# Kernel optimization log

Measured on AMD Instinct MI355X. Metric: run time of the kernel, lower is better.

The kernel has to match this reference:

```python
import jax, jax.numpy as jnp
import numpy as np

TEMP = 0.5
WEIGHT = (0.4, 0.3, 0.3)


def _l2norm(x):
    n = jnp.linalg.norm(x, axis=-1, keepdims=True)
    return x / jnp.maximum(n, 1e-12)


def _forward(st_i, st_j, car_i, car_j, pl_i, pl_j, gt_labels,
             cen_st, cen_car, cen_pl, conc):
    w = jnp.asarray(WEIGHT, dtype=st_i.dtype)[:, None, None]  # [3,1,1]
    feats = [jnp.concatenate([_l2norm(a), _l2norm(b)], axis=0)
             for a, b in ((st_i, st_j), (car_i, car_j), (pl_i, pl_j))]  # each [N,D]
    sims = jnp.stack([f @ f.T for f in feats])  # [3,N,N]
    wmask = jnp.where(sims == 0, jnp.zeros_like(w), w)
    wsim = (sims * wmask).sum(0) / (wmask.sum(0) + 1e-12)  # [N,N]
    e = jnp.exp(wsim / TEMP)
    N = e.shape[0]
    B = N // 2
    idx = jnp.arange(N)
    pos = e[idx, (idx + B) % N]  # positive_mask gather: one positive per row
    # negative_mask excludes diagonal and the positive -> row sum minus both
    neg_sum = e.sum(-1) - e[idx, idx] - pos
    loss = (-jnp.log(pos / (pos + neg_sum))).mean()

    # prototype branch: gt_labels covers all C clusters, unique set == arange(C)
    labels = gt_labels[:, 0]  # [N]
    C = cen_st.shape[0]
    k = jnp.arange(C - 1)
    neg_ids = k[None, :] + (k[None, :] >= labels[:, None]).astype(k.dtype)  # sorted ids != label
    proto_ids = jnp.concatenate([labels[:, None], neg_ids], axis=1)  # [N,C], col 0 = positive
    logits = jnp.stack([
        jnp.take_along_axis(f @ c.T, proto_ids, axis=1)
        for f, c in zip(feats, (cen_st, cen_car, cen_pl))])  # [3,N,C]
    temp_proto = conc[:, proto_ids]  # [3,N,C]
    logits = logits / (temp_proto + 1e-12)
    w2 = jnp.where((temp_proto == 0) | (logits == 0), jnp.zeros_like(w), w)
    logits_w = (logits * w2).sum(0) / (w2.sum(0) + 1e-12)  # [N,C]
    # CrossEntropyLoss(mean) with target class 0 for every row
    loss_proto = (-jax.nn.log_softmax(logits_w, axis=-1)[:, 0]).mean()
    return loss + loss_proto


def setup_inputs() -> dict:
    key = jax.random.key(0)
    ks = jax.random.split(key, 12)
    B, D, C = 2048, 128, 512
    N = 2 * B
    inp = {}
    names = ['st_feat_i', 'st_feat_j', 'car_feat_i', 'car_feat_j',
             'plate_feat_i', 'plate_feat_j']
    for i, nm in enumerate(names):
        inp[nm] = jax.random.normal(ks[i], (B, D), dtype=jnp.float32)
    # labels covering all C clusters so torch.unique(gt_labels) == arange(C)
    labels = jnp.tile(jnp.arange(C, dtype=jnp.int32), N // C)
    labels = jax.random.permutation(ks[6], labels)
    inp['gt_labels'] = labels[:, None]
    inp['st_centroids'] = jax.random.normal(ks[7], (C, D), dtype=jnp.float32)
    inp['car_centroids'] = jax.random.normal(ks[8], (C, D), dtype=jnp.float32)
    inp['plate_centroids'] = jax.random.normal(ks[9], (C, D), dtype=jnp.float32)
    inp['concentration'] = jax.random.uniform(ks[10], (3, C), dtype=jnp.float32,
                                              minval=0.1, maxval=1.0)
    return inp


def reference(st_feat_i, st_feat_j, car_feat_i, car_feat_j,
              plate_feat_i, plate_feat_j, gt_labels,
              st_centroids, car_centroids, plate_centroids, concentration):
    return _forward(st_feat_i, st_feat_j, car_feat_i, car_feat_j,
                    plate_feat_i, plate_feat_j, gt_labels,
                    st_centroids, car_centroids, plate_centroids, concentration)
```

## Files before the change

kernel.cpp:

```cpp
#include <hip/hip_runtime.h>
#include <hip/hip_bf16.h>
#include <math.h>

#define BB 2048
#define NN 4096
#define DD 128
#define CC 512

typedef __attribute__((ext_vector_type(8))) short bf16x8;
typedef __attribute__((ext_vector_type(4))) float f32x4;

__global__ void k_norm(const float* __restrict__ si, const float* __restrict__ sj,
                       const float* __restrict__ ci, const float* __restrict__ cj,
                       const float* __restrict__ pi, const float* __restrict__ pj,
                       __hip_bfloat16* __restrict__ fbf) {
  const int row = blockIdx.x;
  const int m   = blockIdx.y;
  const float* src;
  float sqw;
  if (m == 0)      { src = (row < BB) ? si : sj; sqw = 0.632455532033676f; }
  else if (m == 1) { src = (row < BB) ? ci : cj; sqw = 0.547722557505166f; }
  else             { src = (row < BB) ? pi : pj; sqw = 0.547722557505166f; }
  const int r = (row < BB) ? row : row - BB;
  const float2* s2 = (const float2*)(src + (size_t)r * DD);
  const int t = threadIdx.x;
  float2 v = s2[t];
  float ss = v.x * v.x + v.y * v.y;
  #pragma unroll
  for (int k = 32; k >= 1; k >>= 1) ss += __shfl_xor(ss, k);
  const float inv = sqw / fmaxf(sqrtf(ss), 1e-12f);
  __hip_bfloat16* db = fbf + (size_t)m * NN * DD + (size_t)row * DD;
  db[2 * t]     = __float2bfloat16(v.x * inv);
  db[2 * t + 1] = __float2bfloat16(v.y * inv);
}

__global__ void k_prep(const float* __restrict__ cst, const float* __restrict__ cca,
                       const float* __restrict__ cpl, const float* __restrict__ conc,
                       __hip_bfloat16* __restrict__ cbf) {
  const int row = blockIdx.x;
  const int m   = blockIdx.y;
  const float* src = (m == 0) ? cst : (m == 1) ? cca : cpl;
  const float sqw = (m == 0) ? 0.632455532033676f : 0.547722557505166f;
  const float sc  = sqw / (conc[m * CC + row] + 1e-12f);
  const float2* s2 = (const float2*)(src + (size_t)row * DD);
  const int t = threadIdx.x;
  float2 v = s2[t];
  __hip_bfloat16* db = cbf + (size_t)m * CC * DD + (size_t)row * DD;
  db[2 * t]     = __float2bfloat16(v.x * sc);
  db[2 * t + 1] = __float2bfloat16(v.y * sc);
}

__global__ __launch_bounds__(256, 3) void k_sim(const __hip_bfloat16* __restrict__ fbf,
                                                float* __restrict__ rowsum,
                                                float* __restrict__ pos_e,
                                                float* __restrict__ diag_e) {
  __shared__ bf16x8 As[1024];
  __shared__ bf16x8 Bs[1024];

  int tB = blockIdx.x;
  int by = 0;
  while (tB >= 32 - by) { tB -= 32 - by; ++by; }
  const int bx = by + tB;
  const bool diag = (by == bx);
  const int rowBase = by * 128;
  const int colBase = bx * 128;

  const int tid  = threadIdx.x;
  const int lane = tid & 63;
  const int wid  = tid >> 6;
  const int wr   = wid >> 1, wc = wid & 1;
  const int l15  = lane & 15;
  const int kg   = lane >> 4;

  const int srow = tid >> 3;
  const int kc   = tid & 7;
  const int sc   = kc ^ (srow & 7);

  f32x4 acc[4][4] = {};
  bf16x8 ra[4], rb[4];

  {
    const __hip_bfloat16* F = fbf;
    #pragma unroll
    for (int q = 0; q < 4; ++q) {
      ra[q] = *(const bf16x8*)(F + (size_t)(rowBase + q * 32 + srow) * DD + kc * 8);
      if (!diag)
        rb[q] = *(const bf16x8*)(F + (size_t)(colBase + q * 32 + srow) * DD + kc * 8);
    }
  }

  for (int t = 0; t < 6; ++t) {
    #pragma unroll
    for (int q = 0; q < 4; ++q) {
      As[(q * 32 + srow) * 8 + sc] = ra[q];
      if (!diag) Bs[(q * 32 + srow) * 8 + sc] = rb[q];
    }
    __syncthreads();

    if (t < 5) {
      const __hip_bfloat16* F = fbf + (size_t)((t + 1) >> 1) * NN * DD + ((t + 1) & 1) * 64;
      #pragma unroll
      for (int q = 0; q < 4; ++q) {
        ra[q] = *(const bf16x8*)(F + (size_t)(rowBase + q * 32 + srow) * DD + kc * 8);
        if (!diag)
          rb[q] = *(const bf16x8*)(F + (size_t)(colBase + q * 32 + srow) * DD + kc * 8);
      }
    }

    const bf16x8* Bsrc = diag ? As : Bs;
    #pragma unroll
    for (int ks2 = 0; ks2 < 2; ++ks2) {
      bf16x8 a[4], b[4];
      const int ch = (ks2 * 4 + kg) ^ (l15 & 7);
      #pragma unroll
      for (int ti = 0; ti < 4; ++ti)
        a[ti] = As[(wr * 64 + ti * 16 + l15) * 8 + ch];
      #pragma unroll
      for (int tj = 0; tj < 4; ++tj)
        b[tj] = Bsrc[(wc * 64 + tj * 16 + l15) * 8 + ch];
      #pragma unroll
      for (int ti = 0; ti < 4; ++ti)
        #pragma unroll
        for (int tj = 0; tj < 4; ++tj)
          acc[ti][tj] = __builtin_amdgcn_mfma_f32_16x16x32_bf16(a[ti], b[tj], acc[ti][tj], 0, 0, 0);
    }
    __syncthreads();
  }

  float csum[4] = {0.f, 0.f, 0.f, 0.f};
  #pragma unroll
  for (int ti = 0; ti < 4; ++ti) {
    #pragma unroll
    for (int j = 0; j < 4; ++j) {
      const int i = rowBase + wr * 64 + ti * 16 + kg * 4 + j;
      float rsum = 0.f;
      #pragma unroll
      for (int tj = 0; tj < 4; ++tj) {
        const int jcol = colBase + wc * 64 + tj * 16 + l15;
        const float e = expf(2.0f * acc[ti][tj][j]);
        rsum += e;
        csum[tj] += e;
        if (diag) {
          if (jcol == i) diag_e[i] = e;
        } else if (jcol == ((i + BB) & (NN - 1))) {
          pos_e[i] = e;
          pos_e[jcol] = e;
        }
      }
      #pragma unroll
      for (int msk = 8; msk >= 1; msk >>= 1) rsum += __shfl_xor(rsum, msk);
      if (l15 == 0) atomicAdd(&rowsum[i], rsum);
    }
  }
  if (!diag) {
    #pragma unroll
    for (int tj = 0; tj < 4; ++tj) {
      float v = csum[tj];
      v += __shfl_xor(v, 16);
      v += __shfl_xor(v, 32);
      if (lane < 16) atomicAdd(&rowsum[colBase + wc * 64 + tj * 16 + l15], v);
    }
  }
}

__global__ __launch_bounds__(256) void k_pmm(const __hip_bfloat16* __restrict__ fbf,
                                             const __hip_bfloat16* __restrict__ cbf,
                                             float* __restrict__ Z, int rowOff) {
  const int tid  = threadIdx.x;
  const int lane = tid & 63;
  const int wid  = tid >> 6;
  const int wr   = wid >> 1, wc = wid & 1;
  const int rowBase = rowOff + blockIdx.y * 64 + wr * 32;
  const int colBase = blockIdx.x * 64 + wc * 32;
  const int l15 = lane & 15;
  const int kg  = lane >> 4;

  f32x4 acc[2][2] = {};
  bf16x8 abuf[2][2], bbuf[2][2];

  {
    const int koff = kg * 8;
    #pragma unroll
    for (int ti = 0; ti < 2; ++ti) {
      abuf[0][ti] = *(const bf16x8*)(fbf + (size_t)(rowBase + ti * 16 + l15) * DD + koff);
      bbuf[0][ti] = *(const bf16x8*)(cbf + (size_t)(colBase + ti * 16 + l15) * DD + koff);
    }
  }
  #pragma unroll
  for (int ks = 0; ks < 12; ++ks) {
    const int cur = ks & 1, nxt = cur ^ 1;
    if (ks < 11) {
      const int k1 = ks + 1;
      const int koff = (k1 & 3) * 32 + kg * 8;
      const __hip_bfloat16* F  = fbf + (size_t)(k1 >> 2) * NN * DD + koff;
      const __hip_bfloat16* Cm = cbf + (size_t)(k1 >> 2) * CC * DD + koff;
      #pragma unroll
      for (int ti = 0; ti < 2; ++ti) {
        abuf[nxt][ti] = *(const bf16x8*)(F  + (size_t)(rowBase + ti * 16 + l15) * DD);
        bbuf[nxt][ti] = *(const bf16x8*)(Cm + (size_t)(colBase + ti * 16 + l15) * DD);
      }
    }
    #pragma unroll
    for (int ti = 0; ti < 2; ++ti)
      #pragma unroll
      for (int tj = 0; tj < 2; ++tj)
        acc[ti][tj] = __builtin_amdgcn_mfma_f32_16x16x32_bf16(abuf[cur][ti], bbuf[cur][tj], acc[ti][tj], 0, 0, 0);
  }

  #pragma unroll
  for (int ti = 0; ti < 2; ++ti) {
    #pragma unroll
    for (int j = 0; j < 4; ++j) {
      const int r = rowBase + ti * 16 + kg * 4 + j - rowOff;
      #pragma unroll
      for (int tj = 0; tj < 2; ++tj) {
        const int c = colBase + tj * 16 + l15;
        Z[(size_t)r * CC + c] = acc[ti][tj][j];
      }
    }
  }
}

__global__ __launch_bounds__(256) void k_smax(const float* __restrict__ Z,
                                              const int* __restrict__ labels,
                                              float* __restrict__ lossB, int rowOff) {
  const int tid  = threadIdx.x;
  const int lane = tid & 63;
  const int rloc = blockIdx.x * 4 + (tid >> 6);
  const int row  = rowOff + rloc;
  const float4* zr = (const float4*)(Z + (size_t)rloc * CC);
  const float4 a = zr[lane * 2];
  const float4 b = zr[lane * 2 + 1];
  float mx = fmaxf(fmaxf(fmaxf(a.x, a.y), fmaxf(a.z, a.w)),
                   fmaxf(fmaxf(b.x, b.y), fmaxf(b.z, b.w)));
  #pragma unroll
  for (int k = 32; k >= 1; k >>= 1) mx = fmaxf(mx, __shfl_xor(mx, k));
  float se = expf(a.x - mx) + expf(a.y - mx) + expf(a.z - mx) + expf(a.w - mx)
           + expf(b.x - mx) + expf(b.y - mx) + expf(b.z - mx) + expf(b.w - mx);
  #pragma unroll
  for (int k = 32; k >= 1; k >>= 1) se += __shfl_xor(se, k);
  if (lane == 0) {
    const float zlab = Z[(size_t)rloc * CC + labels[row]];
    lossB[row] = mx + logf(se) - zlab;
  }
}

__global__ void k_final(const float* __restrict__ rowsum, const float* __restrict__ pos_e,
                        const float* __restrict__ diag_e, const float* __restrict__ lossB,
                        float* __restrict__ out) {
  __shared__ float redA[4], redB[4];
  const int tid = threadIdx.x;
  float sa = 0.f, sb = 0.f;
  for (int i = tid; i < NN; i += 256) {
    sa += logf(rowsum[i] - diag_e[i]) - logf(pos_e[i]);
    sb += lossB[i];
  }
  const int lane = tid & 63, wv = tid >> 6;
  #pragma unroll
  for (int k = 32; k >= 1; k >>= 1) { sa += __shfl_xor(sa, k); sb += __shfl_xor(sb, k); }
  if (lane == 0) { redA[wv] = sa; redB[wv] = sb; }
  __syncthreads();
  if (tid == 0) {
    const float la = redA[0] + redA[1] + redA[2] + redA[3];
    const float lb = redB[0] + redB[1] + redB[2] + redB[3];
    out[0] = la / (float)NN + lb / (float)NN;
  }
}

extern "C" void kernel_launch(void* const* d_in, const int* in_sizes, int n_in,
                              void* d_out, int out_size, void* d_ws, size_t ws_size,
                              hipStream_t stream) {
  (void)in_sizes; (void)n_in; (void)out_size; (void)ws_size;
  const float* si  = (const float*)d_in[0];
  const float* sj  = (const float*)d_in[1];
  const float* ci  = (const float*)d_in[2];
  const float* cj  = (const float*)d_in[3];
  const float* pi  = (const float*)d_in[4];
  const float* pj  = (const float*)d_in[5];
  const int*   lab = (const int*)d_in[6];
  const float* cst = (const float*)d_in[7];
  const float* cca = (const float*)d_in[8];
  const float* cpl = (const float*)d_in[9];
  const float* cnc = (const float*)d_in[10];

  float* ws     = (float*)d_ws;
  float* Z      = ws;
  float* rowsum = Z + (size_t)BB * CC;
  float* pos_e  = rowsum + NN;
  float* diag_e = pos_e + NN;
  float* lossB  = diag_e + NN;
  __hip_bfloat16* fbf = (__hip_bfloat16*)(lossB + NN);
  __hip_bfloat16* cbf = fbf + (size_t)3 * NN * DD;

  hipMemsetAsync(rowsum, 0, NN * sizeof(float), stream);

  k_norm<<<dim3(NN, 3), 64, 0, stream>>>(si, sj, ci, cj, pi, pj, fbf);
  k_prep<<<dim3(CC, 3), 64, 0, stream>>>(cst, cca, cpl, cnc, cbf);
  k_sim<<<528, 256, 0, stream>>>(fbf, rowsum, pos_e, diag_e);
  k_pmm<<<dim3(CC / 64, BB / 64), 256, 0, stream>>>(fbf, cbf, Z, 0);
  k_smax<<<BB / 4, 256, 0, stream>>>(Z, lab, lossB, 0);
  k_pmm<<<dim3(CC / 64, BB / 64), 256, 0, stream>>>(fbf, cbf, Z, BB);
  k_smax<<<BB / 4, 256, 0, stream>>>(Z, lab, lossB, BB);
  k_final<<<1, 256, 0, stream>>>(rowsum, pos_e, diag_e, lossB, (float*)d_out);
}
```

Baseline: 134.2 us.

## Fuse prototype matmul with softmax cross-entropy and merge norm/prep kernels

Replaces the two-pass prototype path (matmul writing a logits matrix Z, then a separate softmax pass, run twice over row halves) with one kernel where each block computes 16 rows by all 512 centroids in registers and does the max/sum-exp/label pick in place via shuffles and shared memory. This drops the Z round-trip through global memory and cuts four launches down to one. Separately, the feature normalization and centroid prep kernels are merged into a single launch using 4 rows per 256-thread block. The fused kernel loses the double-buffered loads and launches only 256 blocks, each reading the full centroid set, so latency hiding and occupancy may be weaker.

New measurement: 127.9 us. -4.7%, faster.

```diff
diff --git a/kernel.cpp b/kernel.cpp
--- a/kernel.cpp
+++ b/kernel.cpp
@@ -10,44 +10,42 @@
 typedef __attribute__((ext_vector_type(8))) short bf16x8;
 typedef __attribute__((ext_vector_type(4))) float f32x4;
 
-__global__ void k_norm(const float* __restrict__ si, const float* __restrict__ sj,
-                       const float* __restrict__ ci, const float* __restrict__ cj,
-                       const float* __restrict__ pi, const float* __restrict__ pj,
-                       __hip_bfloat16* __restrict__ fbf) {
-  const int row = blockIdx.x;
+__global__ __launch_bounds__(256) void k_normprep(
+    const float* __restrict__ si, const float* __restrict__ sj,
+    const float* __restrict__ ci, const float* __restrict__ cj,
+    const float* __restrict__ pi, const float* __restrict__ pj,
+    const float* __restrict__ cst, const float* __restrict__ cca,
+    const float* __restrict__ cpl, const float* __restrict__ conc,
+    __hip_bfloat16* __restrict__ fbf, __hip_bfloat16* __restrict__ cbf) {
   const int m   = blockIdx.y;
-  const float* src;
-  float sqw;
-  if (m == 0)      { src = (row < BB) ? si : sj; sqw = 0.632455532033676f; }
-  else if (m == 1) { src = (row < BB) ? ci : cj; sqw = 0.547722557505166f; }
-  else             { src = (row < BB) ? pi : pj; sqw = 0.547722557505166f; }
-  const int r = (row < BB) ? row : row - BB;
-  const float2* s2 = (const float2*)(src + (size_t)r * DD);
-  const int t = threadIdx.x;
-  float2 v = s2[t];
-  float ss = v.x * v.x + v.y * v.y;
-  #pragma unroll
-  for (int k = 32; k >= 1; k >>= 1) ss += __shfl_xor(ss, k);
-  const float inv = sqw / fmaxf(sqrtf(ss), 1e-12f);
-  __hip_bfloat16* db = fbf + (size_t)m * NN * DD + (size_t)row * DD;
-  db[2 * t]     = __float2bfloat16(v.x * inv);
-  db[2 * t + 1] = __float2bfloat16(v.y * inv);
-}
-
-__global__ void k_prep(const float* __restrict__ cst, const float* __restrict__ cca,
-                       const float* __restrict__ cpl, const float* __restrict__ conc,
-                       __hip_bfloat16* __restrict__ cbf) {
-  const int row = blockIdx.x;
-  const int m   = blockIdx.y;
-  const float* src = (m == 0) ? cst : (m == 1) ? cca : cpl;
+  const int tid = threadIdx.x;
+  const int w   = tid >> 6;
+  const int t   = tid & 63;
   const float sqw = (m == 0) ? 0.632455532033676f : 0.547722557505166f;
-  const float sc  = sqw / (conc[m * CC + row] + 1e-12f);
-  const float2* s2 = (const float2*)(src + (size_t)row * DD);
-  const int t = threadIdx.x;
-  float2 v = s2[t];
-  __hip_bfloat16* db = cbf + (size_t)m * CC * DD + (size_t)row * DD;
-  db[2 * t]     = __float2bfloat16(v.x * sc);
-  db[2 * t + 1] = __float2bfloat16(v.y * sc);
+  if (blockIdx.x < NN / 4) {
+    const int row = blockIdx.x * 4 + w;
+    const float* src;
+    if (m == 0)      src = (row < BB) ? si : sj;
+    else if (m == 1) src = (row < BB) ? ci : cj;
+    else             src = (row < BB) ? pi : pj;
+    const int r = (row < BB) ? row : row - BB;
+    float2 v = ((const float2*)(src + (size_t)r * DD))[t];
+    float ss = v.x * v.x + v.y * v.y;
+    #pragma unroll
+    for (int k = 32; k >= 1; k >>= 1) ss += __shfl_xor(ss, k);
+    const float inv = sqw / fmaxf(sqrtf(ss), 1e-12f);
+    __hip_bfloat16* db = fbf + (size_t)m * NN * DD + (size_t)row * DD;
+    db[2 * t]     = __float2bfloat16(v.x * inv);
+    db[2 * t + 1] = __float2bfloat16(v.y * inv);
+  } else {
+    const int crow = (blockIdx.x - NN / 4) * 4 + w;
+    const float* src = (m == 0) ? cst : (m == 1) ? cca : cpl;
+    const float sc = sqw / (conc[m * CC + crow] + 1e-12f);
+    float2 v = ((const float2*)(src + (size_t)crow * DD))[t];
+    __hip_bfloat16* db = cbf + (size_t)m * CC * DD + (size_t)crow * DD;
+    db[2 * t]     = __float2bfloat16(v.x * sc);
+    db[2 * t + 1] = __float2bfloat16(v.y * sc);
+  }
 }
 
 __global__ __launch_bounds__(256, 3) void k_sim(const __hip_bfloat16* __restrict__ fbf,
@@ -163,85 +161,77 @@
   }
 }
 
-__global__ __launch_bounds__(256) void k_pmm(const __hip_bfloat16* __restrict__ fbf,
-                                             const __hip_bfloat16* __restrict__ cbf,
-                                             float* __restrict__ Z, int rowOff) {
+__global__ __launch_bounds__(256) void k_proto2(const __hip_bfloat16* __restrict__ fbf,
+                                                const __hip_bfloat16* __restrict__ cbf,
+                                                const int* __restrict__ labels,
+                                                float* __restrict__ lossB) {
+  __shared__ int   slab[16];
+  __shared__ float wmax[4][16], wsum[4][16], zlab[16];
   const int tid  = threadIdx.x;
   const int lane = tid & 63;
-  const int wid  = tid >> 6;
-  const int wr   = wid >> 1, wc = wid & 1;
-  const int rowBase = rowOff + blockIdx.y * 64 + wr * 32;
-  const int colBase = blockIdx.x * 64 + wc * 32;
-  const int l15 = lane & 15;
-  const int kg  = lane >> 4;
-
-  f32x4 acc[2][2] = {};
-  bf16x8 abuf[2][2], bbuf[2][2];
-
-  {
-    const int koff = kg * 8;
-    #pragma unroll
-    for (int ti = 0; ti < 2; ++ti) {
-      abuf[0][ti] = *(const bf16x8*)(fbf + (size_t)(rowBase + ti * 16 + l15) * DD + koff);
-      bbuf[0][ti] = *(const bf16x8*)(cbf + (size_t)(colBase + ti * 16 + l15) * DD + koff);
-    }
-  }
+  const int w    = tid >> 6;
+  const int l15  = lane & 15;
+  const int kg   = lane >> 4;
+  const int row0 = blockIdx.x * 16;
+
+  if (tid < 16) slab[tid] = labels[row0 + tid];
+  __syncthreads();
+
+  f32x4 acc[8] = {};
   #pragma unroll
   for (int ks = 0; ks < 12; ++ks) {
-    const int cur = ks & 1, nxt = cur ^ 1;
-    if (ks < 11) {
-      const int k1 = ks + 1;
-      const int koff = (k1 & 3) * 32 + kg * 8;
-      const __hip_bfloat16* F  = fbf + (size_t)(k1 >> 2) * NN * DD + koff;
-      const __hip_bfloat16* Cm = cbf + (size_t)(k1 >> 2) * CC * DD + koff;
-      #pragma unroll
-      for (int ti = 0; ti < 2; ++ti) {
-        abuf[nxt][ti] = *(const bf16x8*)(F  + (size_t)(rowBase + ti * 16 + l15) * DD);
-        bbuf[nxt][ti] = *(const bf16x8*)(Cm + (size_t)(colBase + ti * 16 + l15) * DD);
-      }
-    }
-    #pragma unroll
-    for (int ti = 0; ti < 2; ++ti)
-      #pragma unroll
-      for (int tj = 0; tj < 2; ++tj)
-        acc[ti][tj] = __builtin_amdgcn_mfma_f32_16x16x32_bf16(abuf[cur][ti], bbuf[cur][tj], acc[ti][tj], 0, 0, 0);
-  }
-
-  #pragma unroll
-  for (int ti = 0; ti < 2; ++ti) {
-    #pragma unroll
-    for (int j = 0; j < 4; ++j) {
-      const int r = rowBase + ti * 16 + kg * 4 + j - rowOff;
-      #pragma unroll
-      for (int tj = 0; tj < 2; ++tj) {
-        const int c = colBase + tj * 16 + l15;
-        Z[(size_t)r * CC + c] = acc[ti][tj][j];
-      }
-    }
-  }
-}
-
-__global__ __launch_bounds__(256) void k_smax(const float* __restrict__ Z,
-                                              const int* __restrict__ labels,
-                                              float* __restrict__ lossB, int rowOff) {
-  const int tid  = threadIdx.x;
-  const int lane = tid & 63;
-  const int rloc = blockIdx.x * 4 + (tid >> 6);
-  const int row  = rowOff + rloc;
-  const float4* zr = (const float4*)(Z + (size_t)rloc * CC);
-  const float4 a = zr[lane * 2];
-  const float4 b = zr[lane * 2 + 1];
-  float mx = fmaxf(fmaxf(fmaxf(a.x, a.y), fmaxf(a.z, a.w)),
-                   fmaxf(fmaxf(b.x, b.y), fmaxf(b.z, b.w)));
-  #pragma unroll
-  for (int k = 32; k >= 1; k >>= 1) mx = fmaxf(mx, __shfl_xor(mx, k));
-  float se = expf(a.x - mx) + expf(a.y - mx) + expf(a.z - mx) + expf(a.w - mx)
-           + expf(b.x - mx) + expf(b.y - mx) + expf(b.z - mx) + expf(b.w - mx);
-  #pragma unroll
-  for (int k = 32; k >= 1; k >>= 1) se += __shfl_xor(se, k);
-  if (lane == 0) {
-    const float zlab = Z[(size_t)rloc * CC + labels[row]];
-    lossB[row] = mx + logf(se) - zlab;
+    const int koff = (ks & 3) * 32 + kg * 8;
+    const __hip_bfloat16* F  = fbf + (size_t)(ks >> 2) * NN * DD + koff;
+    const __hip_bfloat16* Cm = cbf + (size_t)(ks >> 2) * CC * DD + koff;
+    const bf16x8 af = *(const bf16x8*)(F + (size_t)(row0 + l15) * DD);
+    bf16x8 bf_[8];
+    #pragma unroll
+    for (int tj = 0; tj < 8; ++tj)
+      bf_[tj] = *(const bf16x8*)(Cm + (size_t)(w * 128 + tj * 16 + l15) * DD);
+    #pragma unroll
+    for (int tj = 0; tj < 8; ++tj)
+      acc[tj] = __builtin_amdgcn_mfma_f32_16x16x32_bf16(af, bf_[tj], acc[tj], 0, 0, 0);
+  }
+
+  #pragma unroll
+  for (int j = 0; j < 4; ++j) {
+    const int r = kg * 4 + j;
+    #pragma unroll
+    for (int tj = 0; tj < 8; ++tj) {
+      const int c = w * 128 + tj * 16 + l15;
+      if (c == slab[r]) zlab[r] = acc[tj][j];
+    }
+  }
+
+  #pragma unroll
+  for (int j = 0; j < 4; ++j) {
+    float mx = acc[0][j];
+    #pragma unroll
+    for (int tj = 1; tj < 8; ++tj) mx = fmaxf(mx, acc[tj][j]);
+    #pragma unroll
+    for (int msk = 8; msk >= 1; msk >>= 1) mx = fmaxf(mx, __shfl_xor(mx, msk));
+    if (l15 == 0) wmax[w][kg * 4 + j] = mx;
+  }
+  __syncthreads();
+
+  #pragma unroll
+  for (int j = 0; j < 4; ++j) {
+    const int r = kg * 4 + j;
+    const float bmx = fmaxf(fmaxf(wmax[0][r], wmax[1][r]), fmaxf(wmax[2][r], wmax[3][r]));
+    float se = 0.f;
+    #pragma unroll
+    for (int tj = 0; tj < 8; ++tj) se += expf(acc[tj][j] - bmx);
+    #pragma unroll
+    for (int msk = 8; msk >= 1; msk >>= 1) se += __shfl_xor(se, msk);
+    if (l15 == 0) wsum[w][r] = se;
+  }
+  __syncthreads();
+
+  if (tid < 16) {
+    const int r = tid;
+    const float bmx = fmaxf(fmaxf(wmax[0][r], wmax[1][r]), fmaxf(wmax[2][r], wmax[3][r]));
+    const float s = wsum[0][r] + wsum[1][r] + wsum[2][r] + wsum[3][r];
+    lossB[row0 + r] = bmx + logf(s) - zlab[r];
   }
 }
 
@@ -284,8 +274,7 @@
   const float* cnc = (const float*)d_in[10];
 
   float* ws     = (float*)d_ws;
-  float* Z      = ws;
-  float* rowsum = Z + (size_t)BB * CC;
+  float* rowsum = ws;
   float* pos_e  = rowsum + NN;
   float* diag_e = pos_e + NN;
   float* lossB  = diag_e + NN;
@@ -294,12 +283,9 @@
 
   hipMemsetAsync(rowsum, 0, NN * sizeof(float), stream);
 
-  k_norm<<<dim3(NN, 3), 64, 0, stream>>>(si, sj, ci, cj, pi, pj, fbf);
-  k_prep<<<dim3(CC, 3), 64, 0, stream>>>(cst, cca, cpl, cnc, cbf);
+  k_normprep<<<dim3(NN / 4 + CC / 4, 3), 256, 0, stream>>>(si, sj, ci, cj, pi, pj,
+                                                           cst, cca, cpl, cnc, fbf, cbf);
   k_sim<<<528, 256, 0, stream>>>(fbf, rowsum, pos_e, diag_e);
-  k_pmm<<<dim3(CC / 64, BB / 64), 256, 0, stream>>>(fbf, cbf, Z, 0);
-  k_smax<<<BB / 4, 256, 0, stream>>>(Z, lab, lossB, 0);
-  k_pmm<<<dim3(CC / 64, BB / 64), 256, 0, stream>>>(fbf, cbf, Z, BB);
-  k_smax<<<BB / 4, 256, 0, stream>>>(Z, lab, lossB, BB);
+  k_proto2<<<NN / 16, 256, 0, stream>>>(fbf, cbf, lab, lossB);
   k_final<<<1, 256, 0, stream>>>(rowsum, pos_e, diag_e, lossB, (float*)d_out);
 }
```
